# Kernel optimization log

Hardware: AMD Instinct MI355X
Metric: run time of the kernel (lower is better)

Reference implementation:

```python
import jax, jax.numpy as jnp
import numpy as np

B, C, H, W = 256, 256, 16, 16   # batch, backbone channels, spatial (H*W = 256 = loop count)
E, NCLS = 128, 200              # opt.embed_size, opt.class_num

def _conv(x, w, stride, pad):
    # NCHW / OIHW conv, explicit torch-style symmetric padding
    return jax.lax.conv_general_dilated(x, w, (stride, stride), [(pad, pad), (pad, pad)],
                                        dimension_numbers=('NCHW', 'OIHW', 'NCHW'))

def _bn(x, s, b):
    # eval-mode BatchNorm folded to per-channel scale + shift
    return x * s[None, :, None, None] + b[None, :, None, None]

def setup_inputs() -> dict:
    key = jax.random.key(0)
    ks = jax.random.split(key, 12)
    f = lambda k, shape, scale: jax.random.normal(k, shape, jnp.float32) * scale
    bn_s = lambda k, n: 1.0 + 0.05 * jax.random.normal(k, (n,), jnp.float32)
    bn_b = lambda k, n: 0.05 * jax.random.normal(k, (n,), jnp.float32)
    return {
        'x': f(ks[0], (B, C, H, W), 1.0),
        'embed_w': f(ks[1], (E, C), 0.05),
        'embed_b': f(ks[2], (E,), 0.05),
        'b1_conv1': f(ks[3], (512, 256, 3, 3), 0.03),
        'b1_bn1_s': bn_s(jax.random.fold_in(key, 101), 512),
        'b1_bn1_b': bn_b(jax.random.fold_in(key, 102), 512),
        'b1_conv2': f(ks[4], (512, 512, 3, 3), 0.02),
        'b1_bn2_s': bn_s(jax.random.fold_in(key, 103), 512),
        'b1_bn2_b': bn_b(jax.random.fold_in(key, 104), 512),
        'b1_down_w': f(ks[5], (512, 256, 1, 1), 0.05),
        'b1_down_s': bn_s(jax.random.fold_in(key, 105), 512),
        'b1_down_b': bn_b(jax.random.fold_in(key, 106), 512),
        'b2_conv1': f(ks[6], (512, 512, 3, 3), 0.02),
        'b2_bn1_s': bn_s(jax.random.fold_in(key, 107), 512),
        'b2_bn1_b': bn_b(jax.random.fold_in(key, 108), 512),
        'b2_conv2': f(ks[7], (512, 512, 3, 3), 0.02),
        'b2_bn2_s': bn_s(jax.random.fold_in(key, 109), 512),
        'b2_bn2_b': bn_b(jax.random.fold_in(key, 110), 512),
        'head_w': f(ks[8], (NCLS, 512), 0.05),
    }

def reference(x, embed_w, embed_b,
              b1_conv1, b1_bn1_s, b1_bn1_b, b1_conv2, b1_bn2_s, b1_bn2_b,
              b1_down_w, b1_down_s, b1_down_b,
              b2_conv1, b2_bn1_s, b2_bn1_b, b2_conv2, b2_bn2_s, b2_bn2_b,
              head_w):
    # --- resblock = resnet layer4 (two BasicBlocks, 256->512, stride 2) ---
    y = jax.nn.relu(_bn(_conv(x, b1_conv1, 2, 1), b1_bn1_s, b1_bn1_b))
    y = _bn(_conv(y, b1_conv2, 1, 1), b1_bn2_s, b1_bn2_b)
    sc = _bn(_conv(x, b1_down_w, 2, 0), b1_down_s, b1_down_b)
    y = jax.nn.relu(y + sc)                              # [B,512,8,8]
    z = jax.nn.relu(_bn(_conv(y, b2_conv1, 1, 1), b2_bn1_s, b2_bn1_b))
    z = _bn(_conv(z, b2_conv2, 1, 1), b2_bn2_s, b2_bn2_b)
    z = jax.nn.relu(z + y)
    # --- class prediction: global avg pool + bias-free linear ---
    feat = jnp.mean(z, axis=(2, 3))                      # [B,512]
    prediction = feat @ head_w.T                         # [B,NCLS]
    # --- consistency: 1x1-conv embedding, then pairwise Gram + sigmoid ---
    emb = jnp.einsum('bchw,ec->behw', x, embed_w) + embed_b[None, :, None, None]
    emb = emb.reshape(B, E, H * W)                       # [B,E,256]
    inv_sqrt_e = jnp.float32(1.0 / np.sqrt(E))
    # vol[b,q,i] = sum_c emb[b,c,i]*emb[b,c,q] / sqrt(E)  (matches the 256-iter loop)
    vol = jax.nn.sigmoid(jnp.einsum('bei,beq->bqi', emb, emb) * inv_sqrt_e)
    return (prediction, vol)
```

## Files before the change

### kernel.cpp

```cpp
#include <hip/hip_runtime.h>


using short8 = __attribute__((ext_vector_type(8))) short;
using f32x4  = __attribute__((ext_vector_type(4))) float;
typedef unsigned short u16;
typedef unsigned int   u32;

#define MFMA(a,b,c) __builtin_amdgcn_mfma_f32_16x16x32_bf16((a),(b),(c),0,0,0)

__device__ __forceinline__ u16 f2b(float f){
    u32 u = __builtin_bit_cast(u32, f);
    u += 0x7FFFu + ((u >> 16) & 1u);
    return (u16)(u >> 16);
}
__device__ __forceinline__ float b2f(u16 h){
    u32 u = ((u32)h) << 16;
    return __builtin_bit_cast(float, u);
}
__device__ __forceinline__ u32 pack2(float a, float b){
    return (u32)f2b(a) | ((u32)f2b(b) << 16);
}
__device__ __forceinline__ float sigmoidf_(float v){
    return 1.0f / (1.0f + __expf(-v));
}

__global__ __launch_bounds__(256)
void prep_kernel(const float* __restrict__ w1, const float* __restrict__ s1,
                 const float* __restrict__ w2, const float* __restrict__ s2,
                 const float* __restrict__ w3, const float* __restrict__ s3,
                 const float* __restrict__ w4, const float* __restrict__ s4,
                 const float* __restrict__ wd, const float* __restrict__ sd,
                 const float* __restrict__ ew,
                 u16* __restrict__ wp1, u16* __restrict__ wp2,
                 u16* __restrict__ wp3, u16* __restrict__ wp4,
                 u16* __restrict__ wpd, u16* __restrict__ wpe)
{
    const int N2 = 9*16*512*40, N1 = 9*8*512*40, ND = 8*512*40, NE = 8*128*40;
    int t = blockIdx.x * 256 + threadIdx.x;
    if (t < N2) {
        int j = t % 40; int r = t / 40; int co = r & 511; int q = r >> 9;
        int cc = q & 15; int dydx = q >> 4;
        float v = (j < 32) ? w2[(co*512 + cc*32 + j)*9 + dydx] * s2[co] : 0.f;
        wp2[t] = f2b(v); return;
    }
    t -= N2;
    if (t < N2) {
        int j = t % 40; int r = t / 40; int co = r & 511; int q = r >> 9;
        int cc = q & 15; int dydx = q >> 4;
        float v = (j < 32) ? w3[(co*512 + cc*32 + j)*9 + dydx] * s3[co] : 0.f;
        wp3[t] = f2b(v); return;
    }
    t -= N2;
    if (t < N2) {
        int j = t % 40; int r = t / 40; int co = r & 511; int q = r >> 9;
        int cc = q & 15; int dydx = q >> 4;
        float v = (j < 32) ? w4[(co*512 + cc*32 + j)*9 + dydx] * s4[co] : 0.f;
        wp4[t] = f2b(v); return;
    }
    t -= N2;
    if (t < N1) {
        int j = t % 40; int r = t / 40; int co = r & 511; int q = r >> 9;
        int cc = q & 7; int dydx = q >> 3;
        float v = (j < 32) ? w1[(co*256 + cc*32 + j)*9 + dydx] * s1[co] : 0.f;
        wp1[t] = f2b(v); return;
    }
    t -= N1;
    if (t < ND) {
        int j = t % 40; int r = t / 40; int co = r & 511; int cc = r >> 9;
        float v = (j < 32) ? wd[co*256 + cc*32 + j] * sd[co] : 0.f;
        wpd[t] = f2b(v); return;
    }
    t -= ND;
    if (t < NE) {
        int j = t % 40; int r = t / 40; int e = r & 127; int cc = r >> 7;
        float v = (j < 32) ? ew[e*256 + cc*32 + j] : 0.f;
        wpe[t] = f2b(v);
    }
}

__global__ __launch_bounds__(512, 2)
void conv1_kernel(const float* __restrict__ x, const u16* __restrict__ wp,
                  const float* __restrict__ bnb, u16* __restrict__ out)
{
    const int cot = blockIdx.x;
    const int b0  = blockIdx.y * 2;
    const int tid = threadIdx.x;
    const int wid = tid >> 6, lane = tid & 63;
    const int ln = lane & 15, kg = lane >> 4;
    const int wco = wid >> 1;
    const int bb  = wid & 1;

    __shared__ u16 actb[2][2*289*40];

    {
        short8 zz = {0,0,0,0,0,0,0,0};
        short8* ab = (short8*)&actb[0][0];
        for (int j = tid; j < 2*2*289*40/8; j += 512) ab[j] = zz;
    }
    __syncthreads();

    auto stage_act = [&](int cc, int p){
        #pragma unroll
        for (int it = 0; it < 16; ++it){
            int f = it*512 + tid;
            int bb2 = f >> 12; int rem = f & 4095;
            int cip = rem >> 8; int px = rem & 255;
            const float* src = &x[(((size_t)(b0+bb2)*256 + cc*32 + 2*cip)*256) + px];
            float v0 = src[0], v1 = src[256];
            int r = ((px >> 4) + 1)*17 + (px & 15) + 1;
            *(u32*)&actb[p][(bb2*289 + r)*40 + 2*cip] = pack2(v0, v1);
        }
    };

    stage_act(0, 0);
    __syncthreads();

    f32x4 zero4 = {0.f,0.f,0.f,0.f};
    f32x4 acc[4][4];
    #pragma unroll
    for (int mf = 0; mf < 4; ++mf)
        #pragma unroll
        for (int nf = 0; nf < 4; ++nf) acc[mf][nf] = zero4;

    int bbase[4];
    #pragma unroll
    for (int nf = 0; nf < 4; ++nf){
        int px = nf*16 + ln;
        bbase[nf] = (bb*289 + 34*(px>>3) + 2*(px&7))*40 + kg*8;
    }

    for (int cc = 0; cc < 8; ++cc){
        if (cc < 7) stage_act(cc+1, (cc+1) & 1);
        const u16* abp = actb[cc & 1];
        #pragma unroll
        for (int d = 0; d < 9; ++d){
            const u16* wdp = wp + ((size_t)(d*8 + cc)*512 + cot*256)*40;
            int dy = d/3, dx = d - dy*3;
            int shift = (dy*17 + dx)*40;
            short8 A[4];
            #pragma unroll
            for (int mf = 0; mf < 4; ++mf)
                A[mf] = *(const short8*)&wdp[(wco*64 + mf*16 + ln)*40 + kg*8];
            #pragma unroll
            for (int nf = 0; nf < 4; ++nf){
                short8 B = *(const short8*)&abp[bbase[nf] + shift];
                #pragma unroll
                for (int mf = 0; mf < 4; ++mf)
                    acc[mf][nf] = MFMA(A[mf], B, acc[mf][nf]);
            }
        }
        __syncthreads();
    }

    #pragma unroll
    for (int mf = 0; mf < 4; ++mf){
        int co0 = cot*256 + wco*64 + mf*16 + kg*4;
        float4 bv = *(const float4*)&bnb[co0];
        #pragma unroll
        for (int nf = 0; nf < 4; ++nf){
            int px = nf*16 + ln;
            size_t o = (((size_t)(b0+bb)*64) + px)*512 + co0;
            f32x4 a = acc[mf][nf];
            ushort4 st;
            st.x = f2b(fmaxf(a[0] + bv.x, 0.f));
            st.y = f2b(fmaxf(a[1] + bv.y, 0.f));
            st.z = f2b(fmaxf(a[2] + bv.z, 0.f));
            st.w = f2b(fmaxf(a[3] + bv.w, 0.f));
            *(ushort4*)&out[o] = st;
        }
    }
}

template<int DOWN, int RES>
__global__ __launch_bounds__(64, 2)
void conv_s1_kernel(const u16* __restrict__ in, const u16* __restrict__ wp,
                    const float* __restrict__ bnb,
                    const float* __restrict__ x, const u16* __restrict__ wpd,
                    const float* __restrict__ dbb,
                    const u16* __restrict__ res, u16* __restrict__ out)
{
    const int bid = blockIdx.x;
    const int cot = (bid >> 3) & 7;
    const int b   = (bid & 7) | ((bid >> 6) << 3);
    const int lane = threadIdx.x;
    const int ln = lane & 15, kg = lane >> 4;

    __shared__ u16 actb[2][3232];

    {
        short8 zz = {0,0,0,0,0,0,0,0};
        short8* ab = (short8*)&actb[0][0];
        #pragma unroll
        for (int it = 0; it < 13; ++it){
            int j = it*64 + lane;
            if (j < 808) ab[j] = zz;
        }
    }

    int s_ld[4]; size_t s_go[4];
    #pragma unroll
    for (int it = 0; it < 4; ++it){
        int j = it*64 + lane;
        int px = j >> 2, cg = j & 3;
        int row = ((px>>3)+1)*10 + (px&7) + 1;
        s_ld[it] = cg*808 + row*8;
        s_go[it] = (((size_t)b*64 + px)*512) + cg*8;
    }

    short8 sreg[4];
    auto stage_load = [&](int cc){
        #pragma unroll
        for (int it = 0; it < 4; ++it)
            sreg[it] = *(const short8*)&in[s_go[it] + cc*32];
    };
    auto stage_store = [&](int p){
        #pragma unroll
        for (int it = 0; it < 4; ++it)
            *(short8*)&actb[p][s_ld[it]] = sreg[it];
    };

    stage_load(0); stage_store(0);

    f32x4 zero4 = {0.f,0.f,0.f,0.f};
    f32x4 acc[4][4];
    #pragma unroll
    for (int mf = 0; mf < 4; ++mf)
        #pragma unroll
        for (int nf = 0; nf < 4; ++nf) acc[mf][nf] = zero4;

    int bro[4];
    #pragma unroll
    for (int nf = 0; nf < 4; ++nf){
        int px = nf*16 + ln;
        bro[nf] = kg*808 + ((px>>3)*10 + (px&7))*8;
    }
    const int aoff = ln*40 + kg*8;
    const int abase = cot*64*40;

    for (int cc = 0; cc < 16; ++cc){
        if (cc < 15) stage_load(cc+1);
        const u16* abp = actb[cc & 1];
        #pragma unroll
        for (int dy = 0; dy < 3; ++dy){
            short8 A[3][4];
            #pragma unroll
            for (int dx = 0; dx < 3; ++dx){
                const u16* wdp = wp + (size_t)((dy*3+dx)*16 + cc)*512*40 + abase;
                #pragma unroll
                for (int mf = 0; mf < 4; ++mf)
                    A[dx][mf] = *(const short8*)&wdp[mf*640 + aoff];
            }
            #pragma unroll
            for (int dx = 0; dx < 3; ++dx){
                int shift = (dy*10 + dx)*8;
                #pragma unroll
                for (int nf = 0; nf < 4; ++nf){
                    short8 B = *(const short8*)&abp[bro[nf] + shift];
                    #pragma unroll
                    for (int mf = 0; mf < 4; ++mf)
                        acc[mf][nf] = MFMA(A[dx][mf], B, acc[mf][nf]);
                }
            }
        }
        if (cc < 15) stage_store((cc+1) & 1);
    }

    if (DOWN){
        for (int dc = 0; dc < 8; ++dc){
            #pragma unroll
            for (int it = 0; it < 16; ++it){
                int f = it*64 + lane;
                int cip = f >> 6, px2 = f & 63;
                int ipx = (px2>>3)*32 + (px2&7)*2;
                const float* src = &x[(((size_t)b*256 + dc*32 + 2*cip)*256) + ipx];
                *(u32*)&actb[0][(cip>>2)*808 + px2*8 + (cip&3)*2] = pack2(src[0], src[256]);
            }
            const u16* wdp = wpd + (size_t)(dc*512)*40 + abase;
            short8 A[4];
            #pragma unroll
            for (int mf = 0; mf < 4; ++mf)
                A[mf] = *(const short8*)&wdp[mf*640 + aoff];
            #pragma unroll
            for (int nf = 0; nf < 4; ++nf){
                int rd = nf*16 + ln;
                short8 B = *(const short8*)&actb[0][kg*808 + rd*8];
                #pragma unroll
                for (int mf = 0; mf < 4; ++mf)
                    acc[mf][nf] = MFMA(A[mf], B, acc[mf][nf]);
            }
        }
    }

    #pragma unroll
    for (int mf = 0; mf < 4; ++mf){
        int co0 = cot*64 + mf*16 + kg*4;
        float4 bv = *(const float4*)&bnb[co0];
        if (DOWN){
            float4 dv = *(const float4*)&dbb[co0];
            bv.x += dv.x; bv.y += dv.y; bv.z += dv.z; bv.w += dv.w;
        }
        #pragma unroll
        for (int nf = 0; nf < 4; ++nf){
            int px = nf*16 + ln;
            size_t o = (((size_t)b*64) + px)*512 + co0;
            f32x4 a = acc[mf][nf];
            float v0 = a[0] + bv.x, v1 = a[1] + bv.y;
            float v2 = a[2] + bv.z, v3 = a[3] + bv.w;
            if (RES){
                ushort4 rv = *(const ushort4*)&res[o];
                v0 += b2f(rv.x); v1 += b2f(rv.y); v2 += b2f(rv.z); v3 += b2f(rv.w);
            }
            ushort4 st;
            st.x = f2b(fmaxf(v0, 0.f)); st.y = f2b(fmaxf(v1, 0.f));
            st.z = f2b(fmaxf(v2, 0.f)); st.w = f2b(fmaxf(v3, 0.f));
            *(ushort4*)&out[o] = st;
        }
    }
}

__global__ __launch_bounds__(256)
void head_kernel(const u16* __restrict__ z, const float* __restrict__ hw,
                 float* __restrict__ pred)
{
    const int b = blockIdx.x, tid = threadIdx.x;
    __shared__ float feat[512];
    float s0 = 0.f, s1 = 0.f;
    for (int px = 0; px < 64; ++px){
        u32 u = *(const u32*)&z[(((size_t)b*64 + px)*512) + 2*tid];
        s0 += b2f((u16)(u & 0xFFFF));
        s1 += b2f((u16)(u >> 16));
    }
    feat[2*tid]   = s0 * (1.f/64.f);
    feat[2*tid+1] = s1 * (1.f/64.f);
    __syncthreads();
    if (tid < 200){
        float acc = 0.f;
        const float4* hp = (const float4*)&hw[(size_t)tid*512];
        #pragma unroll 8
        for (int i = 0; i < 128; ++i){
            float4 h = hp[i];
            float4 f = *(const float4*)&feat[i*4];
            acc += h.x*f.x + h.y*f.y + h.z*f.z + h.w*f.w;
        }
        pred[b*200 + tid] = acc;
    }
}

__global__ __launch_bounds__(512, 2)
void gram_kernel(const float* __restrict__ x, const u16* __restrict__ wpe,
                 const float* __restrict__ eb, float* __restrict__ vol)
{
    const int b = blockIdx.x, tid = threadIdx.x;
    const int wid = tid >> 6, lane = tid & 63;
    const int ln = lane & 15, kg = lane >> 4;

    __shared__ u16 embl[256*136];
    __shared__ u16 xbl[256*40];
    __shared__ u16 ewl[128*40];

    f32x4 zero4 = {0.f,0.f,0.f,0.f};
    f32x4 ae[8][2];
    #pragma unroll
    for (int mf = 0; mf < 8; ++mf){ ae[mf][0] = zero4; ae[mf][1] = zero4; }

    for (int cc = 0; cc < 8; ++cc){
        __syncthreads();
        #pragma unroll
        for (int it = 0; it < 8; ++it){
            int f = it*512 + tid;
            int cip = f >> 8, px = f & 255;
            const float* src = &x[(((size_t)b*256 + cc*32 + 2*cip)*256) + px];
            *(u32*)&xbl[px*40 + 2*cip] = pack2(src[0], src[256]);
        }
        for (int j = tid; j < 640; j += 512)
            *(short8*)&ewl[j*8] = *(const short8*)&wpe[(cc*128)*40 + j*8];
        __syncthreads();
        short8 A[8];
        #pragma unroll
        for (int mf = 0; mf < 8; ++mf)
            A[mf] = *(const short8*)&ewl[(mf*16 + ln)*40 + kg*8];
        #pragma unroll
        for (int nf = 0; nf < 2; ++nf){
            short8 B = *(const short8*)&xbl[(wid*32 + nf*16 + ln)*40 + kg*8];
            #pragma unroll
            for (int mf = 0; mf < 8; ++mf)
                ae[mf][nf] = MFMA(A[mf], B, ae[mf][nf]);
        }
    }
    #pragma unroll
    for (int mf = 0; mf < 8; ++mf){
        int e0 = mf*16 + kg*4;
        float4 bv = *(const float4*)&eb[e0];
        #pragma unroll
        for (int nf = 0; nf < 2; ++nf){
            int px = wid*32 + nf*16 + ln;
            f32x4 a = ae[mf][nf];
            ushort4 st;
            st.x = f2b(a[0] + bv.x); st.y = f2b(a[1] + bv.y);
            st.z = f2b(a[2] + bv.z); st.w = f2b(a[3] + bv.w);
            *(ushort4*)&embl[px*136 + e0] = st;
        }
    }
    __syncthreads();

    const int wq = wid >> 2, wi = wid & 3;
    f32x4 g[8][4];
    #pragma unroll
    for (int mf = 0; mf < 8; ++mf)
        #pragma unroll
        for (int nf = 0; nf < 4; ++nf) g[mf][nf] = zero4;

    #pragma unroll
    for (int ks = 0; ks < 4; ++ks){
        short8 A[8];
        #pragma unroll
        for (int mf = 0; mf < 8; ++mf)
            A[mf] = *(const short8*)&embl[(wq*128 + mf*16 + ln)*136 + ks*32 + kg*8];
        #pragma unroll
        for (int nf = 0; nf < 4; ++nf){
            short8 B = *(const short8*)&embl[(wi*64 + nf*16 + ln)*136 + ks*32 + kg*8];
            #pragma unroll
            for (int mf = 0; mf < 8; ++mf)
                g[mf][nf] = MFMA(A[mf], B, g[mf][nf]);
        }
    }
    const float sc = 0.08838834764831845f;
    #pragma unroll
    for (int mf = 0; mf < 8; ++mf){
        #pragma unroll
        for (int nf = 0; nf < 4; ++nf){
            int i = wi*64 + nf*16 + ln;
            #pragma unroll
            for (int r = 0; r < 4; ++r){
                int q = wq*128 + mf*16 + kg*4 + r;
                vol[(((size_t)b*256 + q)*256) + i] = sigmoidf_(g[mf][nf][r] * sc);
            }
        }
    }
}

extern "C" void kernel_launch(void* const* d_in, const int* in_sizes, int n_in,
                              void* d_out, int out_size, void* d_ws, size_t ws_size,
                              hipStream_t stream)
{
    const float* x    = (const float*)d_in[0];
    const float* ew   = (const float*)d_in[1];
    const float* eb   = (const float*)d_in[2];
    const float* w1   = (const float*)d_in[3];
    const float* bn1s = (const float*)d_in[4];
    const float* bn1b = (const float*)d_in[5];
    const float* w2   = (const float*)d_in[6];
    const float* bn2s = (const float*)d_in[7];
    const float* bn2b = (const float*)d_in[8];
    const float* wd   = (const float*)d_in[9];
    const float* bnds = (const float*)d_in[10];
    const float* bndb = (const float*)d_in[11];
    const float* w3   = (const float*)d_in[12];
    const float* bn3s = (const float*)d_in[13];
    const float* bn3b = (const float*)d_in[14];
    const float* w4   = (const float*)d_in[15];
    const float* bn4s = (const float*)d_in[16];
    const float* bn4b = (const float*)d_in[17];
    const float* hw   = (const float*)d_in[18];

    float* pred = (float*)d_out;
    float* vol  = pred + 51200;

    u16* wp2 = (u16*)d_ws;
    u16* wp3 = wp2 + 2949120;
    u16* wp4 = wp3 + 2949120;
    u16* wp1 = wp4 + 2949120;
    u16* wpd = wp1 + 1474560;
    u16* wpe = wpd + 163840;

    u16* y1 = (u16*)vol;
    u16* y  = y1 + 8388608;
    u16* z1 = y  + 8388608;
    u16* z  = z1 + 8388608;

    prep_kernel<<<41120, 256, 0, stream>>>(w1, bn1s, w2, bn2s, w3, bn3s, w4, bn4s,
                                           wd, bnds, ew, wp1, wp2, wp3, wp4, wpd, wpe);
    conv1_kernel<<<dim3(2,128), 512, 0, stream>>>(x, wp1, bn1b, y1);
    conv_s1_kernel<1,0><<<2048, 64, 0, stream>>>(y1, wp2, bn2b, x, wpd, bndb,
                                                 nullptr, y);
    conv_s1_kernel<0,0><<<2048, 64, 0, stream>>>(y, wp3, bn3b, nullptr, nullptr,
                                                 nullptr, nullptr, z1);
    conv_s1_kernel<0,1><<<2048, 64, 0, stream>>>(z1, wp4, bn4b, nullptr, nullptr,
                                                 nullptr, y, z);
    head_kernel<<<256, 256, 0, stream>>>(z, hw, pred);
    gram_kernel<<<256, 512, 0, stream>>>(x, wpe, eb, vol);
}
```

Measured before the change: 384.9 us.

## Split conv K-loop across two waves per block with LDS reduction

Each conv_s1 block now uses two waves that each process half of the input-channel chunks (and half of the downsample chunks) into private LDS buffers. The second wave's partial accumulators are written to LDS as bf16 and summed by the first wave in the epilogue. This aims to raise wave-level parallelism and latency hiding per output tile. It drops per-wave double buffering, adds two block barriers, and rounds partial sums to bf16, which costs some accuracy.

```diff
diff --git a/kernel.cpp b/kernel.cpp
--- a/kernel.cpp
+++ b/kernel.cpp
@@ -172,7 +172,7 @@
 }
 
 template<int DOWN, int RES>
-__global__ __launch_bounds__(64, 2)
+__global__ __launch_bounds__(128, 3)
 void conv_s1_kernel(const u16* __restrict__ in, const u16* __restrict__ wp,
                     const float* __restrict__ bnb,
                     const float* __restrict__ x, const u16* __restrict__ wpd,
@@ -182,18 +182,21 @@
     const int bid = blockIdx.x;
     const int cot = (bid >> 3) & 7;
     const int b   = (bid & 7) | ((bid >> 6) << 3);
-    const int lane = threadIdx.x;
+    const int tid = threadIdx.x;
+    const int w   = tid >> 6;
+    const int lane = tid & 63;
     const int ln = lane & 15, kg = lane >> 4;
 
-    __shared__ u16 actb[2][3232];
+    __shared__ u16 actb[6464];
+    const int wb = w * 3232;
 
     {
         short8 zz = {0,0,0,0,0,0,0,0};
-        short8* ab = (short8*)&actb[0][0];
-        #pragma unroll
-        for (int it = 0; it < 13; ++it){
+        short8* ab = (short8*)&actb[wb];
+        #pragma unroll
+        for (int it = 0; it < 7; ++it){
             int j = it*64 + lane;
-            if (j < 808) ab[j] = zz;
+            if (j < 404) ab[j] = zz;
         }
     }
 
@@ -203,7 +206,7 @@
         int j = it*64 + lane;
         int px = j >> 2, cg = j & 3;
         int row = ((px>>3)+1)*10 + (px&7) + 1;
-        s_ld[it] = cg*808 + row*8;
+        s_ld[it] = wb + cg*808 + row*8;
         s_go[it] = (((size_t)b*64 + px)*512) + cg*8;
     }
 
@@ -213,13 +216,14 @@
         for (int it = 0; it < 4; ++it)
             sreg[it] = *(const short8*)&in[s_go[it] + cc*32];
     };
-    auto stage_store = [&](int p){
+    auto stage_store = [&](){
         #pragma unroll
         for (int it = 0; it < 4; ++it)
-            *(short8*)&actb[p][s_ld[it]] = sreg[it];
+            *(short8*)&actb[s_ld[it]] = sreg[it];
     };
 
-    stage_load(0); stage_store(0);
+    const int cbase = w * 8;
+    stage_load(cbase); stage_store();
 
     f32x4 zero4 = {0.f,0.f,0.f,0.f};
     f32x4 acc[4][4];
@@ -232,14 +236,14 @@
     #pragma unroll
     for (int nf = 0; nf < 4; ++nf){
         int px = nf*16 + ln;
-        bro[nf] = kg*808 + ((px>>3)*10 + (px&7))*8;
+        bro[nf] = wb + kg*808 + ((px>>3)*10 + (px&7))*8;
     }
     const int aoff = ln*40 + kg*8;
     const int abase = cot*64*40;
 
-    for (int cc = 0; cc < 16; ++cc){
-        if (cc < 15) stage_load(cc+1);
-        const u16* abp = actb[cc & 1];
+    for (int lc = 0; lc < 8; ++lc){
+        const int cc = cbase + lc;
+        if (lc < 7) stage_load(cc+1);
         #pragma unroll
         for (int dy = 0; dy < 3; ++dy){
             short8 A[3][4];
@@ -255,25 +259,26 @@
                 int shift = (dy*10 + dx)*8;
                 #pragma unroll
                 for (int nf = 0; nf < 4; ++nf){
-                    short8 B = *(const short8*)&abp[bro[nf] + shift];
+                    short8 B = *(const short8*)&actb[bro[nf] + shift];
                     #pragma unroll
                     for (int mf = 0; mf < 4; ++mf)
                         acc[mf][nf] = MFMA(A[dx][mf], B, acc[mf][nf]);
                 }
             }
         }
-        if (cc < 15) stage_store((cc+1) & 1);
+        if (lc < 7) stage_store();
     }
 
     if (DOWN){
-        for (int dc = 0; dc < 8; ++dc){
+        for (int ld = 0; ld < 4; ++ld){
+            const int dc = w*4 + ld;
             #pragma unroll
             for (int it = 0; it < 16; ++it){
                 int f = it*64 + lane;
                 int cip = f >> 6, px2 = f & 63;
                 int ipx = (px2>>3)*32 + (px2&7)*2;
                 const float* src = &x[(((size_t)b*256 + dc*32 + 2*cip)*256) + ipx];
-                *(u32*)&actb[0][(cip>>2)*808 + px2*8 + (cip&3)*2] = pack2(src[0], src[256]);
+                *(u32*)&actb[wb + (cip>>2)*808 + px2*8 + (cip&3)*2] = pack2(src[0], src[256]);
             }
             const u16* wdp = wpd + (size_t)(dc*512)*40 + abase;
             short8 A[4];
@@ -283,7 +288,7 @@
             #pragma unroll
             for (int nf = 0; nf < 4; ++nf){
                 int rd = nf*16 + ln;
-                short8 B = *(const short8*)&actb[0][kg*808 + rd*8];
+                short8 B = *(const short8*)&actb[wb + kg*808 + rd*8];
                 #pragma unroll
                 for (int mf = 0; mf < 4; ++mf)
                     acc[mf][nf] = MFMA(A[mf], B, acc[mf][nf]);
@@ -291,29 +296,51 @@
         }
     }
 
-    #pragma unroll
-    for (int mf = 0; mf < 4; ++mf){
-        int co0 = cot*64 + mf*16 + kg*4;
-        float4 bv = *(const float4*)&bnb[co0];
-        if (DOWN){
-            float4 dv = *(const float4*)&dbb[co0];
-            bv.x += dv.x; bv.y += dv.y; bv.z += dv.z; bv.w += dv.w;
-        }
-        #pragma unroll
-        for (int nf = 0; nf < 4; ++nf){
-            int px = nf*16 + ln;
-            size_t o = (((size_t)b*64) + px)*512 + co0;
-            f32x4 a = acc[mf][nf];
-            float v0 = a[0] + bv.x, v1 = a[1] + bv.y;
-            float v2 = a[2] + bv.z, v3 = a[3] + bv.w;
-            if (RES){
-                ushort4 rv = *(const ushort4*)&res[o];
-                v0 += b2f(rv.x); v1 += b2f(rv.y); v2 += b2f(rv.z); v3 += b2f(rv.w);
-            }
-            ushort4 st;
-            st.x = f2b(fmaxf(v0, 0.f)); st.y = f2b(fmaxf(v1, 0.f));
-            st.z = f2b(fmaxf(v2, 0.f)); st.w = f2b(fmaxf(v3, 0.f));
-            *(ushort4*)&out[o] = st;
+    __syncthreads();
+    if (w == 1){
+        #pragma unroll
+        for (int mf = 0; mf < 4; ++mf){
+            int co0 = mf*16 + kg*4;
+            #pragma unroll
+            for (int nf = 0; nf < 4; ++nf){
+                int px = nf*16 + ln;
+                f32x4 a = acc[mf][nf];
+                ushort4 st;
+                st.x = f2b(a[0]); st.y = f2b(a[1]);
+                st.z = f2b(a[2]); st.w = f2b(a[3]);
+                *(ushort4*)&actb[px*64 + co0] = st;
+            }
+        }
+    }
+    __syncthreads();
+    if (w == 0){
+        #pragma unroll
+        for (int mf = 0; mf < 4; ++mf){
+            int co0 = cot*64 + mf*16 + kg*4;
+            float4 bv = *(const float4*)&bnb[co0];
+            if (DOWN){
+                float4 dv = *(const float4*)&dbb[co0];
+                bv.x += dv.x; bv.y += dv.y; bv.z += dv.z; bv.w += dv.w;
+            }
+            #pragma unroll
+            for (int nf = 0; nf < 4; ++nf){
+                int px = nf*16 + ln;
+                ushort4 pv = *(const ushort4*)&actb[px*64 + mf*16 + kg*4];
+                size_t o = (((size_t)b*64) + px)*512 + co0;
+                f32x4 a = acc[mf][nf];
+                float v0 = a[0] + b2f(pv.x) + bv.x;
+                float v1 = a[1] + b2f(pv.y) + bv.y;
+                float v2 = a[2] + b2f(pv.z) + bv.z;
+                float v3 = a[3] + b2f(pv.w) + bv.w;
+                if (RES){
+                    ushort4 rv = *(const ushort4*)&res[o];
+                    v0 += b2f(rv.x); v1 += b2f(rv.y); v2 += b2f(rv.z); v3 += b2f(rv.w);
+                }
+                ushort4 st;
+                st.x = f2b(fmaxf(v0, 0.f)); st.y = f2b(fmaxf(v1, 0.f));
+                st.z = f2b(fmaxf(v2, 0.f)); st.w = f2b(fmaxf(v3, 0.f));
+                *(ushort4*)&out[o] = st;
+            }
         }
     }
 }
@@ -481,12 +508,12 @@
     prep_kernel<<<41120, 256, 0, stream>>>(w1, bn1s, w2, bn2s, w3, bn3s, w4, bn4s,
                                            wd, bnds, ew, wp1, wp2, wp3, wp4, wpd, wpe);
     conv1_kernel<<<dim3(2,128), 512, 0, stream>>>(x, wp1, bn1b, y1);
-    conv_s1_kernel<1,0><<<2048, 64, 0, stream>>>(y1, wp2, bn2b, x, wpd, bndb,
-                                                 nullptr, y);
-    conv_s1_kernel<0,0><<<2048, 64, 0, stream>>>(y, wp3, bn3b, nullptr, nullptr,
-                                                 nullptr, nullptr, z1);
-    conv_s1_kernel<0,1><<<2048, 64, 0, stream>>>(z1, wp4, bn4b, nullptr, nullptr,
-                                                 nullptr, y, z);
+    conv_s1_kernel<1,0><<<2048, 128, 0, stream>>>(y1, wp2, bn2b, x, wpd, bndb,
+                                                  nullptr, y);
+    conv_s1_kernel<0,0><<<2048, 128, 0, stream>>>(y, wp3, bn3b, nullptr, nullptr,
+                                                  nullptr, nullptr, z1);
+    conv_s1_kernel<0,1><<<2048, 128, 0, stream>>>(z1, wp4, bn4b, nullptr, nullptr,
+                                                  nullptr, y, z);
     head_kernel<<<256, 256, 0, stream>>>(z, hw, pred);
     gram_kernel<<<256, 512, 0, stream>>>(x, wpe, eb, vol);
 }
```

Result: slower. 434.0 us (+12.8%).
